# Kernel optimization log

Hardware: AMD Instinct MI355X
Metric: run time of the kernel (lower is better)

Reference implementation:

```python
import jax, jax.numpy as jnp
import numpy as np

IN_DIM = 64
OUT_DIM = 64
NUM_HEADS = 4
NEG_SLOPE = 0.2
GAMMA = 1.0  # constraint_gamma
NUM_VARS = 100000
NUM_CLAUSES = 100000
NUM_CLUSTERS = 2048
VARS_PER = 64
CLAUSES_PER = 64
NUM_EDGES = 400000


def _xavier(k, shape):
    bound = np.sqrt(6.0 / (shape[0] + shape[1])).astype(np.float32)
    return jax.random.uniform(k, shape, jnp.float32, -bound, bound)


def setup_inputs() -> dict:
    key = jax.random.key(0)
    ks = jax.random.split(key, 11)
    return {
        "x_var": jax.random.normal(ks[0], (NUM_VARS, IN_DIM), jnp.float32),
        "x_clause": jax.random.normal(ks[1], (NUM_CLAUSES, IN_DIM), jnp.float32),
        "var_clause_edge_index": jax.random.randint(ks[2], (2, NUM_EDGES), 0, NUM_VARS),
        "edge_polarity": jax.random.normal(ks[3], (NUM_EDGES, 1), jnp.float32),
        "cluster_var_ids": jax.random.randint(ks[4], (NUM_CLUSTERS, VARS_PER), 0, NUM_VARS),
        "cluster_clause_ids": jax.random.randint(ks[5], (NUM_CLUSTERS, CLAUSES_PER), 0, NUM_CLAUSES),
        "satisfaction_scores": jax.random.uniform(ks[6], (NUM_CLAUSES,), jnp.float32),
        "active_heads": 4,
        "W_Q": _xavier(ks[7], (OUT_DIM, IN_DIM)),
        "W_K": _xavier(ks[8], (OUT_DIM, IN_DIM)),
        "W_V": _xavier(ks[9], (OUT_DIM, IN_DIM)),
        "head_weights": jnp.ones((NUM_HEADS,), jnp.float32),
        "out_proj_w": _xavier(ks[10], (OUT_DIM, OUT_DIM)),
        "out_proj_b": jnp.zeros((OUT_DIM,), jnp.float32),
    }


def reference(x_var, x_clause, var_clause_edge_index, edge_polarity,
              cluster_var_ids, cluster_clause_ids, satisfaction_scores,
              active_heads, W_Q, W_K, W_V, head_weights, out_proj_w, out_proj_b):
    # NOTE: var_clause_edge_index / edge_polarity are accepted but unused,
    # matching the original forward body.
    num_vars = x_var.shape[0]
    x_all = jnp.concatenate([x_var, x_clause], axis=0)            # [N, D]
    Q = x_all @ W_Q.T
    K = x_all @ W_K.T
    V = x_all @ W_V.T

    # Block-diagonal cluster layout: [C, S] with S = VARS_PER + CLAUSES_PER
    nodes = jnp.concatenate([cluster_var_ids, cluster_clause_ids + num_vars], axis=1)
    Qc = Q[nodes]                                                 # [C, S, D]
    Kc = K[nodes]
    Vc = V[nodes]

    scale = jnp.asarray(np.sqrt(OUT_DIM), Qc.dtype)
    scores = jnp.einsum('csd,ctd->cst', Qc, Kc) / scale            # [C, S, S]
    # constraint-aware bias on clause columns (added before leaky_relu)
    bias = jnp.concatenate(
        [jnp.zeros(cluster_var_ids.shape, scores.dtype),
         GAMMA * satisfaction_scores[cluster_clause_ids]], axis=1)  # [C, S]
    scores = jax.nn.leaky_relu(scores + bias[:, None, :], NEG_SLOPE)
    attn = jax.nn.softmax(scores, axis=-1)

    head_w = jnp.mean(head_weights[:active_heads])
    h = jnp.einsum('cst,ctd->csd', attn, Vc) * head_w             # [C, S, D]

    flat = nodes.reshape(-1)
    out = jnp.zeros_like(x_all).at[flat].add(h.reshape(-1, OUT_DIM))
    count = jnp.zeros((x_all.shape[0],), x_all.dtype).at[flat].add(1.0)
    out = out / jnp.maximum(count, 1.0)[:, None]
    out = out @ out_proj_w.T + out_proj_b

    return (x_var + out[:num_vars], x_clause + out[num_vars:])
```

## Files before the change

kernel.cpp:

```cpp
#include <hip/hip_runtime.h>


#define NV 100000
#define NN 200000
#define NCLUST 2048
#define XS 72
#define AS 136

typedef __attribute__((ext_vector_type(8))) short short8;
typedef __attribute__((ext_vector_type(16))) float floatx16;

__device__ __forceinline__ unsigned short f2bf(float f) {
    union { float f; unsigned u; } v; v.f = f;
    unsigned r = v.u + 0x7fffu + ((v.u >> 16) & 1u);
    return (unsigned short)(r >> 16);
}
__device__ __forceinline__ int crow(int r, int lane) {
    return (r & 3) + 8 * (r >> 2) + 4 * (lane >> 5);
}

__global__ __launch_bounds__(256) void prep_kernel(
    const float* __restrict__ WQ, const float* __restrict__ WK,
    const float* __restrict__ WV, const float* __restrict__ Wout,
    const float* __restrict__ head_weights, const int* __restrict__ active_heads_p,
    unsigned short* __restrict__ Mtr, unsigned short* __restrict__ Pbf)
{
    int o = blockIdx.x * blockDim.x + threadIdx.x;
    int ah = active_heads_p[0];
    float hw = 0.f;
    for (int i = 0; i < ah; ++i) hw += head_weights[i];
    hw /= (float)ah;
    if (o < 4096) {
        int d = o >> 6, a = o & 63;
        float acc = 0.f;
        for (int j = 0; j < 64; ++j) acc += WQ[j*64 + a] * WK[j*64 + d];
        Mtr[o] = f2bf(acc * 0.125f);
    } else if (o < 8192) {
        int o2 = o - 4096;
        int j = o2 >> 6, b = o2 & 63;
        float acc = 0.f;
        for (int d = 0; d < 64; ++d) acc += Wout[j*64 + d] * WV[d*64 + b];
        Pbf[o2] = f2bf(acc * hw);
    }
}

__global__ __launch_bounds__(256, 3) void attn_kernel(
    const float* __restrict__ x_var, const float* __restrict__ x_clause,
    const int* __restrict__ cvar, const int* __restrict__ ccl,
    const float* __restrict__ sat, const unsigned short* __restrict__ Mtr,
    unsigned short* __restrict__ accum_bf, float* __restrict__ countv)
{
    __shared__ union {
        struct { unsigned short Zc[128 * XS]; unsigned short Xc[128 * XS]; } s;
        unsigned short attn[128 * AS];
    } u;
    __shared__ unsigned short XcT[64 * AS];

    const int tid = threadIdx.x, lane = tid & 63, w = tid >> 6;
    const int c = blockIdx.x;
    const int m = lane & 31, hk = (lane >> 5) * 8;

    short8 mb0[4], mb1[4];
    #pragma unroll
    for (int ks = 0; ks < 4; ++ks) {
        mb0[ks] = *(const short8*)(Mtr + m * 64 + ks * 16 + hk);
        mb1[ks] = *(const short8*)(Mtr + (32 + m) * 64 + ks * 16 + hk);
    }

    {
        const int r = tid >> 1, half = tid & 1;
        int nid;
        const float* src;
        if (r < 64) {
            nid = cvar[c * 64 + r];
            src = x_var + (size_t)nid * 64;
        } else {
            int cid = ccl[c * 64 + (r - 64)];
            nid = NV + cid;
            src = x_clause + (size_t)cid * 64;
            if (half) *(float*)&XcT[(r - 64) * AS + 132] = sat[cid];
        }
        if (!half) ((int*)&XcT[(r >> 1) * AS + 128])[r & 1] = nid;
        union { unsigned short us[32]; short8 v[4]; } hb;
        const float4* s4 = (const float4*)src + half * 8;
        #pragma unroll
        for (int i = 0; i < 8; ++i) {
            float4 v = s4[i];
            hb.us[i*4+0] = f2bf(v.x); hb.us[i*4+1] = f2bf(v.y);
            hb.us[i*4+2] = f2bf(v.z); hb.us[i*4+3] = f2bf(v.w);
        }
        const int c0 = half * 32;
        #pragma unroll
        for (int i = 0; i < 4; ++i) *(short8*)&u.s.Xc[r * XS + c0 + i * 8] = hb.v[i];
        #pragma unroll
        for (int i = 0; i < 32; ++i) XcT[(c0 + i) * AS + r] = hb.us[i];
    }
    __syncthreads();
    if (tid < 128)
        atomicAdd(&countv[((const int*)&XcT[(tid >> 1) * AS + 128])[tid & 1]], 1.0f);

    floatx16 z0 = {}, z1 = {};
    #pragma unroll
    for (int ks = 0; ks < 4; ++ks) {
        short8 a = *(const short8*)&u.s.Xc[(w * 32 + m) * XS + ks * 16 + hk];
        z0 = __builtin_amdgcn_mfma_f32_32x32x16_bf16(a, mb0[ks], z0, 0, 0, 0);
        z1 = __builtin_amdgcn_mfma_f32_32x32x16_bf16(a, mb1[ks], z1, 0, 0, 0);
    }
    #pragma unroll
    for (int r = 0; r < 16; ++r) {
        int row = w * 32 + crow(r, lane);
        u.s.Zc[row * XS + m]      = f2bf(z0[r]);
        u.s.Zc[row * XS + 32 + m] = f2bf(z1[r]);
    }

    floatx16 sc[4] = {{}, {}, {}, {}};
    #pragma unroll
    for (int ks = 0; ks < 4; ++ks) {
        short8 a = *(const short8*)&u.s.Zc[(w * 32 + m) * XS + ks * 16 + hk];
        #pragma unroll
        for (int nt = 0; nt < 4; ++nt) {
            short8 b = *(const short8*)&u.s.Xc[(nt * 32 + m) * XS + ks * 16 + hk];
            sc[nt] = __builtin_amdgcn_mfma_f32_32x32x16_bf16(a, b, sc[nt], 0, 0, 0);
        }
    }

    const float b2 = *(const float*)&XcT[m * AS + 132];
    const float b3 = *(const float*)&XcT[(32 + m) * AS + 132];
    #pragma unroll
    for (int r = 0; r < 16; ++r) {
        float a0 = sc[0][r], a1 = sc[1][r], a2 = sc[2][r] + b2, a3 = sc[3][r] + b3;
        a0 = a0 > 0.f ? a0 : 0.2f * a0;
        a1 = a1 > 0.f ? a1 : 0.2f * a1;
        a2 = a2 > 0.f ? a2 : 0.2f * a2;
        a3 = a3 > 0.f ? a3 : 0.2f * a3;
        sc[0][r] = __expf(a0); sc[1][r] = __expf(a1);
        sc[2][r] = __expf(a2); sc[3][r] = __expf(a3);
    }

    __syncthreads();

    #pragma unroll
    for (int r = 0; r < 16; ++r) {
        int row = w * 32 + crow(r, lane);
        u.attn[row * AS + m]      = f2bf(sc[0][r]);
        u.attn[row * AS + 32 + m] = f2bf(sc[1][r]);
        u.attn[row * AS + 64 + m] = f2bf(sc[2][r]);
        u.attn[row * AS + 96 + m] = f2bf(sc[3][r]);
    }

    const short8 vones = (short8)(short)0x3F80;
    floatx16 g0 = {}, g1 = {}, rs = {};
    #pragma unroll
    for (int ks = 0; ks < 8; ++ks) {
        short8 a  = *(const short8*)&u.attn[(w * 32 + m) * AS + ks * 16 + hk];
        short8 b0 = *(const short8*)&XcT[m * AS + ks * 16 + hk];
        short8 b1 = *(const short8*)&XcT[(32 + m) * AS + ks * 16 + hk];
        g0 = __builtin_amdgcn_mfma_f32_32x32x16_bf16(a, b0, g0, 0, 0, 0);
        g1 = __builtin_amdgcn_mfma_f32_32x32x16_bf16(a, b1, g1, 0, 0, 0);
        rs = __builtin_amdgcn_mfma_f32_32x32x16_bf16(a, vones, rs, 0, 0, 0);
    }

    const bool ev = !(lane & 1);
    const int colbase = ev ? m : (31 + m);
    #pragma unroll
    for (int r = 0; r < 16; ++r) {
        int row = w * 32 + crow(r, lane);
        int nid = ((const int*)&XcT[(row >> 1) * AS + 128])[row & 1];
        float inv = __builtin_amdgcn_rcpf(rs[r]);
        float a0 = g0[r] * inv, a1 = g1[r] * inv;
        float t0 = __shfl_xor(a0, 1, 64);
        float t1 = __shfl_xor(a1, 1, 64);
        float lo = ev ? a0 : t1;
        float hi = ev ? t0 : a1;
        unsigned pk = (unsigned)f2bf(lo) | ((unsigned)f2bf(hi) << 16);
        unsigned long long addr =
            (unsigned long long)(accum_bf + (size_t)nid * 64 + colbase);
        asm volatile("global_atomic_pk_add_bf16 %0, %1, off"
                     :: "v"(addr), "v"(pk) : "memory");
    }
}

__global__ __launch_bounds__(256, 4) void finalize_kernel(
    const float* __restrict__ x_var, const float* __restrict__ x_clause,
    const unsigned short* __restrict__ accum_bf, const float* __restrict__ countv,
    const unsigned short* __restrict__ Pbf, const float* __restrict__ bout,
    float* __restrict__ out)
{
    __shared__ float cnts[256];
    const int tid = threadIdx.x, lane = tid & 63, w = tid >> 6;
    const int base = blockIdx.x * 256;
    {
        int n = base + tid;
        cnts[tid] = (n < NN) ? countv[n] : 1.f;
    }
    __syncthreads();

    const int m = lane & 31, hk = (lane >> 5) * 8;
    short8 pb[2][4];
    #pragma unroll
    for (int nt = 0; nt < 2; ++nt)
        #pragma unroll
        for (int ks = 0; ks < 4; ++ks)
            pb[nt][ks] = *(const short8*)(Pbf + (nt * 32 + m) * 64 + ks * 16 + hk);
    const float bias0 = bout[m], bias1 = bout[32 + m];

    #pragma unroll
    for (int tm = 0; tm < 2; ++tm) {
        int mt = w * 2 + tm;
        const unsigned short* arow = accum_bf + (size_t)(base + mt * 32 + m) * 64;
        floatx16 c0 = {}, c1 = {};
        #pragma unroll
        for (int ks = 0; ks < 4; ++ks) {
            short8 a = *(const short8*)(arow + ks * 16 + hk);
            c0 = __builtin_amdgcn_mfma_f32_32x32x16_bf16(a, pb[0][ks], c0, 0, 0, 0);
            c1 = __builtin_amdgcn_mfma_f32_32x32x16_bf16(a, pb[1][ks], c1, 0, 0, 0);
        }
        #pragma unroll
        for (int r = 0; r < 16; ++r) {
            int lrow = mt * 32 + crow(r, lane);
            int n = base + lrow;
            if (n < NN) {
                float inv = 1.0f / fmaxf(cnts[lrow], 1.0f);
                const float* xs = (n < NV) ? (x_var + (size_t)n * 64)
                                           : (x_clause + (size_t)(n - NV) * 64);
                out[(size_t)n * 64 + m]      = xs[m]      + c0[r] * inv + bias0;
                out[(size_t)n * 64 + 32 + m] = xs[32 + m] + c1[r] * inv + bias1;
            }
        }
    }
}

extern "C" void kernel_launch(void* const* d_in, const int* in_sizes, int n_in,
                              void* d_out, int out_size, void* d_ws, size_t ws_size,
                              hipStream_t stream)
{
    const float* x_var        = (const float*)d_in[0];
    const float* x_clause     = (const float*)d_in[1];
    const int*   cvar         = (const int*)d_in[4];
    const int*   ccl          = (const int*)d_in[5];
    const float* sat          = (const float*)d_in[6];
    const int*   active_heads = (const int*)d_in[7];
    const float* WQ           = (const float*)d_in[8];
    const float* WK           = (const float*)d_in[9];
    const float* WV           = (const float*)d_in[10];
    const float* head_weights = (const float*)d_in[11];
    const float* Wout         = (const float*)d_in[12];
    const float* bout         = (const float*)d_in[13];

    unsigned short* accum_bf = (unsigned short*)d_ws;
    float* countv = (float*)(accum_bf + (size_t)NN * 64);
    unsigned short* Mtr = (unsigned short*)(countv + NN);
    unsigned short* Pbf = Mtr + 4096;

    hipMemsetAsync(accum_bf, 0, (size_t)NN * 64 * 2 + (size_t)NN * 4, stream);
    prep_kernel<<<32, 256, 0, stream>>>(WQ, WK, WV, Wout, head_weights, active_heads, Mtr, Pbf);
    attn_kernel<<<NCLUST, 256, 0, stream>>>(x_var, x_clause, cvar, ccl, sat, Mtr, accum_bf, countv);
    finalize_kernel<<<(NN + 255) / 256, 256, 0, stream>>>(x_var, x_clause, accum_bf, countv, Pbf, bout, (float*)d_out);
}
```

Before: 214.6 us.

## Shrink attention LDS footprint by dropping transposed copy and reusing score buffer

Removes the transposed XcT shared-memory copy and the 128-wide attention buffer. Softmax row sums are now computed with wave shuffles, and P·V is done in two 64-column halves through a reused 64-wide buffer. The V operand is gathered with strided scalar LDS reads, and the Mtr fragments are loaded inside the loop rather than held in registers. The smaller LDS footprint and lower register pressure are meant to allow 4 blocks per CU instead of 3. In exchange it adds shuffle reductions, strided LDS reads and an extra buffer round-trip.

```diff
diff --git a/kernel.cpp b/kernel.cpp
--- a/kernel.cpp
+++ b/kernel.cpp
@@ -5,7 +5,6 @@
 #define NN 200000
 #define NCLUST 2048
 #define XS 72
-#define AS 136
 
 typedef __attribute__((ext_vector_type(8))) short short8;
 typedef __attribute__((ext_vector_type(16))) float floatx16;
@@ -44,28 +43,20 @@
     }
 }
 
-__global__ __launch_bounds__(256, 3) void attn_kernel(
+__global__ __launch_bounds__(256, 4) void attn_kernel(
     const float* __restrict__ x_var, const float* __restrict__ x_clause,
     const int* __restrict__ cvar, const int* __restrict__ ccl,
     const float* __restrict__ sat, const unsigned short* __restrict__ Mtr,
     unsigned short* __restrict__ accum_bf, float* __restrict__ countv)
 {
-    __shared__ union {
-        struct { unsigned short Zc[128 * XS]; unsigned short Xc[128 * XS]; } s;
-        unsigned short attn[128 * AS];
-    } u;
-    __shared__ unsigned short XcT[64 * AS];
+    __shared__ unsigned short Xc[128 * XS];
+    __shared__ unsigned short Eh[128 * XS];
+    __shared__ int   ids[128];
+    __shared__ float biascl[64];
 
     const int tid = threadIdx.x, lane = tid & 63, w = tid >> 6;
     const int c = blockIdx.x;
     const int m = lane & 31, hk = (lane >> 5) * 8;
-
-    short8 mb0[4], mb1[4];
-    #pragma unroll
-    for (int ks = 0; ks < 4; ++ks) {
-        mb0[ks] = *(const short8*)(Mtr + m * 64 + ks * 16 + hk);
-        mb1[ks] = *(const short8*)(Mtr + (32 + m) * 64 + ks * 16 + hk);
-    }
 
     {
         const int r = tid >> 1, half = tid & 1;
@@ -78,9 +69,9 @@
             int cid = ccl[c * 64 + (r - 64)];
             nid = NV + cid;
             src = x_clause + (size_t)cid * 64;
-            if (half) *(float*)&XcT[(r - 64) * AS + 132] = sat[cid];
-        }
-        if (!half) ((int*)&XcT[(r >> 1) * AS + 128])[r & 1] = nid;
+            if (half) biascl[r - 64] = sat[cid];
+        }
+        if (!half) ids[r] = nid;
         union { unsigned short us[32]; short8 v[4]; } hb;
         const float4* s4 = (const float4*)src + half * 8;
         #pragma unroll
@@ -91,41 +82,41 @@
         }
         const int c0 = half * 32;
         #pragma unroll
-        for (int i = 0; i < 4; ++i) *(short8*)&u.s.Xc[r * XS + c0 + i * 8] = hb.v[i];
-        #pragma unroll
-        for (int i = 0; i < 32; ++i) XcT[(c0 + i) * AS + r] = hb.us[i];
+        for (int i = 0; i < 4; ++i) *(short8*)&Xc[r * XS + c0 + i * 8] = hb.v[i];
     }
     __syncthreads();
-    if (tid < 128)
-        atomicAdd(&countv[((const int*)&XcT[(tid >> 1) * AS + 128])[tid & 1]], 1.0f);
-
-    floatx16 z0 = {}, z1 = {};
+    if (tid < 128) atomicAdd(&countv[ids[tid]], 1.0f);
+
+    {
+        floatx16 z0 = {}, z1 = {};
+        #pragma unroll
+        for (int ks = 0; ks < 4; ++ks) {
+            short8 mb0 = *(const short8*)(Mtr + m * 64 + ks * 16 + hk);
+            short8 mb1 = *(const short8*)(Mtr + (32 + m) * 64 + ks * 16 + hk);
+            short8 a = *(const short8*)&Xc[(w * 32 + m) * XS + ks * 16 + hk];
+            z0 = __builtin_amdgcn_mfma_f32_32x32x16_bf16(a, mb0, z0, 0, 0, 0);
+            z1 = __builtin_amdgcn_mfma_f32_32x32x16_bf16(a, mb1, z1, 0, 0, 0);
+        }
+        #pragma unroll
+        for (int r = 0; r < 16; ++r) {
+            int row = w * 32 + crow(r, lane);
+            Eh[row * XS + m]      = f2bf(z0[r]);
+            Eh[row * XS + 32 + m] = f2bf(z1[r]);
+        }
+    }
+
+    floatx16 sc[4] = {{}, {}, {}, {}};
     #pragma unroll
     for (int ks = 0; ks < 4; ++ks) {
-        short8 a = *(const short8*)&u.s.Xc[(w * 32 + m) * XS + ks * 16 + hk];
-        z0 = __builtin_amdgcn_mfma_f32_32x32x16_bf16(a, mb0[ks], z0, 0, 0, 0);
-        z1 = __builtin_amdgcn_mfma_f32_32x32x16_bf16(a, mb1[ks], z1, 0, 0, 0);
-    }
-    #pragma unroll
-    for (int r = 0; r < 16; ++r) {
-        int row = w * 32 + crow(r, lane);
-        u.s.Zc[row * XS + m]      = f2bf(z0[r]);
-        u.s.Zc[row * XS + 32 + m] = f2bf(z1[r]);
-    }
-
-    floatx16 sc[4] = {{}, {}, {}, {}};
-    #pragma unroll
-    for (int ks = 0; ks < 4; ++ks) {
-        short8 a = *(const short8*)&u.s.Zc[(w * 32 + m) * XS + ks * 16 + hk];
+        short8 a = *(const short8*)&Eh[(w * 32 + m) * XS + ks * 16 + hk];
         #pragma unroll
         for (int nt = 0; nt < 4; ++nt) {
-            short8 b = *(const short8*)&u.s.Xc[(nt * 32 + m) * XS + ks * 16 + hk];
+            short8 b = *(const short8*)&Xc[(nt * 32 + m) * XS + ks * 16 + hk];
             sc[nt] = __builtin_amdgcn_mfma_f32_32x32x16_bf16(a, b, sc[nt], 0, 0, 0);
         }
     }
 
-    const float b2 = *(const float*)&XcT[m * AS + 132];
-    const float b3 = *(const float*)&XcT[(32 + m) * AS + 132];
+    const float b2 = biascl[m], b3 = biascl[32 + m];
     #pragma unroll
     for (int r = 0; r < 16; ++r) {
         float a0 = sc[0][r], a1 = sc[1][r], a2 = sc[2][r] + b2, a3 = sc[3][r] + b3;
@@ -133,31 +124,56 @@
         a1 = a1 > 0.f ? a1 : 0.2f * a1;
         a2 = a2 > 0.f ? a2 : 0.2f * a2;
         a3 = a3 > 0.f ? a3 : 0.2f * a3;
-        sc[0][r] = __expf(a0); sc[1][r] = __expf(a1);
-        sc[2][r] = __expf(a2); sc[3][r] = __expf(a3);
-    }
-
-    __syncthreads();
+        a0 = __expf(a0); a1 = __expf(a1); a2 = __expf(a2); a3 = __expf(a3);
+        float s4 = (a0 + a1) + (a2 + a3);
+        #pragma unroll
+        for (int off = 1; off < 32; off <<= 1) s4 += __shfl_xor(s4, off, 64);
+        float inv = __builtin_amdgcn_rcpf(s4);
+        sc[0][r] = a0 * inv; sc[1][r] = a1 * inv;
+        sc[2][r] = a2 * inv; sc[3][r] = a3 * inv;
+    }
 
     #pragma unroll
     for (int r = 0; r < 16; ++r) {
         int row = w * 32 + crow(r, lane);
-        u.attn[row * AS + m]      = f2bf(sc[0][r]);
-        u.attn[row * AS + 32 + m] = f2bf(sc[1][r]);
-        u.attn[row * AS + 64 + m] = f2bf(sc[2][r]);
-        u.attn[row * AS + 96 + m] = f2bf(sc[3][r]);
-    }
-
-    const short8 vones = (short8)(short)0x3F80;
-    floatx16 g0 = {}, g1 = {}, rs = {};
-    #pragma unroll
-    for (int ks = 0; ks < 8; ++ks) {
-        short8 a  = *(const short8*)&u.attn[(w * 32 + m) * AS + ks * 16 + hk];
-        short8 b0 = *(const short8*)&XcT[m * AS + ks * 16 + hk];
-        short8 b1 = *(const short8*)&XcT[(32 + m) * AS + ks * 16 + hk];
+        Eh[row * XS + m]      = f2bf(sc[0][r]);
+        Eh[row * XS + 32 + m] = f2bf(sc[1][r]);
+    }
+
+    floatx16 g0 = {}, g1 = {};
+    #pragma unroll
+    for (int ks = 0; ks < 4; ++ks) {
+        short8 a = *(const short8*)&Eh[(w * 32 + m) * XS + ks * 16 + hk];
+        short8 b0, b1;
+        #pragma unroll
+        for (int j = 0; j < 8; ++j) {
+            int t = ks * 16 + hk + j;
+            b0[j] = (short)Xc[t * XS + m];
+            b1[j] = (short)Xc[t * XS + 32 + m];
+        }
         g0 = __builtin_amdgcn_mfma_f32_32x32x16_bf16(a, b0, g0, 0, 0, 0);
         g1 = __builtin_amdgcn_mfma_f32_32x32x16_bf16(a, b1, g1, 0, 0, 0);
-        rs = __builtin_amdgcn_mfma_f32_32x32x16_bf16(a, vones, rs, 0, 0, 0);
+    }
+
+    #pragma unroll
+    for (int r = 0; r < 16; ++r) {
+        int row = w * 32 + crow(r, lane);
+        Eh[row * XS + m]      = f2bf(sc[2][r]);
+        Eh[row * XS + 32 + m] = f2bf(sc[3][r]);
+    }
+
+    #pragma unroll
+    for (int ks = 0; ks < 4; ++ks) {
+        short8 a = *(const short8*)&Eh[(w * 32 + m) * XS + ks * 16 + hk];
+        short8 b0, b1;
+        #pragma unroll
+        for (int j = 0; j < 8; ++j) {
+            int t = 64 + ks * 16 + hk + j;
+            b0[j] = (short)Xc[t * XS + m];
+            b1[j] = (short)Xc[t * XS + 32 + m];
+        }
+        g0 = __builtin_amdgcn_mfma_f32_32x32x16_bf16(a, b0, g0, 0, 0, 0);
+        g1 = __builtin_amdgcn_mfma_f32_32x32x16_bf16(a, b1, g1, 0, 0, 0);
     }
 
     const bool ev = !(lane & 1);
@@ -165,9 +181,8 @@
     #pragma unroll
     for (int r = 0; r < 16; ++r) {
         int row = w * 32 + crow(r, lane);
-        int nid = ((const int*)&XcT[(row >> 1) * AS + 128])[row & 1];
-        float inv = __builtin_amdgcn_rcpf(rs[r]);
-        float a0 = g0[r] * inv, a1 = g1[r] * inv;
+        int nid = ids[row];
+        float a0 = g0[r], a1 = g1[r];
         float t0 = __shfl_xor(a0, 1, 64);
         float t1 = __shfl_xor(a1, 1, 64);
         float lo = ev ? a0 : t1;
```

Measured after the change: 213.6 us. About the same (-0.5%).
